# Kernel tuning notes

Hardware: AMD Instinct MI355X
Metric: run time of the kernel (lower is better)

## Reference

```python
import jax, jax.numpy as jnp
import numpy as np

CAPACITY_FACTOR = 1.0  # fairseq Top1Gate default


def setup_inputs() -> dict:
    key = jax.random.key(0)
    ks = jax.random.split(key, 5)
    B, T, M, H, O, E = 8, 1024, 1024, 4096, 1024, 4
    return {
        "hidden_states": jax.random.normal(ks[0], (B, T, M), jnp.float32),
        "gate_w": jax.random.normal(ks[1], (M, E), jnp.float32) * 0.02,
        "fc1_w": jax.random.normal(ks[2], (E, M, H), jnp.float32) * 0.02,
        "fc1_b": jnp.zeros((E, H), jnp.float32),
        "fc2_w": jax.random.normal(ks[3], (E, H, O), jnp.float32) * 0.02,
        "fc2_b": jnp.zeros((E, O), jnp.float32),
    }


def reference(hidden_states, gate_w, fc1_w, fc1_b, fc2_w, fc2_b):
    B, T, M = hidden_states.shape
    E = gate_w.shape[1]
    S = B * T
    C = int(CAPACITY_FACTOR * -(-S // E))  # ceil(S/E)

    features = hidden_states.reshape(S, M)  # [S, M]

    # ---- Top1 gate (fairseq top1gating, eval path: no shuffle/noise) ----
    logits = features @ gate_w                      # [S, E]
    gates = jax.nn.softmax(logits, axis=1)          # [S, E]
    idx = jnp.argmax(gates, axis=1)                 # [S]
    mask1 = jax.nn.one_hot(idx, E, dtype=gates.dtype)  # [S, E]

    # load-balancing aux loss (computed before capacity dropping)
    me = jnp.mean(gates, axis=0)
    ce = jnp.mean(mask1, axis=0)
    l_aux = jnp.sum(me * ce) * E

    # capacity: position within each expert's queue; drop overflow tokens
    locations = jnp.cumsum(mask1, axis=0) - 1.0     # [S, E]
    mask1 = mask1 * (locations < C)
    loc_s = jnp.sum(locations * mask1, axis=1).astype(jnp.int32)  # [S]
    gates1_s = jnp.sum(gates * mask1, axis=1)       # [S] gate value (0 if dropped)

    # combine_weights [S, E, C] and boolean dispatch mask (as float for mm)
    combine = (gates1_s[:, None, None] * mask1[:, :, None]
               * jax.nn.one_hot(loc_s, C, dtype=gates.dtype)[:, None, :])
    dispatch = (combine > 0).astype(features.dtype)  # [S, E, C]

    # ---- dispatch via dense one-hot matmul: [E*C, S] @ [S, M] ----
    dispatch_ecs = jnp.transpose(dispatch, (1, 2, 0)).reshape(E * C, S)
    dispatched = (dispatch_ecs @ features).reshape(E, C, M)

    # ---- per-expert MLP (grouped GEMM) ----
    h = jax.nn.gelu(jnp.einsum('ecm,emh->ech', dispatched, fc1_w) + fc1_b[:, None, :])
    expert_out = jnp.einsum('ech,eho->eco', h, fc2_w) + fc2_b[:, None, :]  # [E, C, O]

    # ---- combine via dense matmul: [S, E*C] @ [E*C, O] ----
    O = expert_out.shape[-1]
    combined = combine.reshape(S, E * C) @ expert_out.reshape(E * C, O)

    return combined.reshape(B, T, O), l_aux
```

## Files before the change

### kernel.cpp

```cpp
#include <hip/hip_runtime.h>
#include <stdint.h>

#define S_TOK 8192
#define MDIM  1024
#define HDIM  4096
#define ODIM  1024
#define NEXP  4
#define CAP   2048

typedef __attribute__((ext_vector_type(8))) short short8;
typedef __attribute__((ext_vector_type(4))) float floatx4;

__device__ __forceinline__ unsigned short f2bf(float x) {
  union { float f; unsigned u; } v; v.f = x;
  unsigned r = v.u + 0x7FFFu + ((v.u >> 16) & 1u);
  return (unsigned short)(r >> 16);
}

__device__ __forceinline__ void gl_lds16(const void* g, void* l) {
  __builtin_amdgcn_global_load_lds(
      (const __attribute__((address_space(1))) void*)g,
      (__attribute__((address_space(3))) void*)l, 16, 0, 0);
}

__device__ __forceinline__ float gelu_tanh(float x) {
  float z = 0.7978845608028654f * (x + 0.044715f * x * x * x);
  float t = 1.0f - 2.0f / (__expf(2.0f * z) + 1.0f);
  return 0.5f * x * (1.0f + t);
}

__global__ __launch_bounds__(256) void gate_kernel(
    const float* __restrict__ feat, const float* __restrict__ gw,
    int* __restrict__ idx, float* __restrict__ gval, float* __restrict__ gsum)
{
  int wave = threadIdx.x >> 6, lane = threadIdx.x & 63;
  int s = blockIdx.x * 4 + wave;
  const float* f = feat + (size_t)s * MDIM;
  double a0 = 0, a1 = 0, a2 = 0, a3 = 0;
  #pragma unroll
  for (int j = 0; j < 16; ++j) {
    int m = lane + j * 64;
    float x = f[m];
    float4 w = ((const float4*)gw)[m];
    a0 += (double)x * w.x; a1 += (double)x * w.y;
    a2 += (double)x * w.z; a3 += (double)x * w.w;
  }
  #pragma unroll
  for (int off = 32; off; off >>= 1) {
    a0 += __shfl_down(a0, off); a1 += __shfl_down(a1, off);
    a2 += __shfl_down(a2, off); a3 += __shfl_down(a3, off);
  }
  __shared__ float bs[4];
  if (threadIdx.x < 4) bs[threadIdx.x] = 0.f;
  __syncthreads();
  if (lane == 0) {
    double lg[4] = {a0, a1, a2, a3};
    double mx = lg[0]; int bi = 0;
    #pragma unroll
    for (int e = 1; e < 4; ++e) if (lg[e] > mx) { mx = lg[e]; bi = e; }
    float ex[4]; float den = 0.f;
    #pragma unroll
    for (int e = 0; e < 4; ++e) { ex[e] = __expf((float)(lg[e] - mx)); den += ex[e]; }
    float inv = 1.f / den;
    idx[s]  = bi;
    gval[s] = ex[bi] * inv;
    #pragma unroll
    for (int e = 0; e < 4; ++e) atomicAdd(&bs[e], ex[e] * inv);
  }
  __syncthreads();
  if (threadIdx.x < 4) atomicAdd(&gsum[threadIdx.x], bs[threadIdx.x]);
}

__global__ __launch_bounds__(1024) void scan_kernel(
    const int* __restrict__ idx, int* __restrict__ perm,
    int* __restrict__ ne, const float* __restrict__ gsum,
    float* __restrict__ laux)
{
  const int tid = threadIdx.x, wave = tid >> 6, lane = tid & 63;
  __shared__ int cnt[16][4];
  __shared__ int off[16][4];
  __shared__ int tot[4];
  unsigned long long below = (lane == 0) ? 0ull : ((~0ull) >> (64 - lane));

  int myE[8], loc[8];
  int c[4] = {0, 0, 0, 0};
  #pragma unroll
  for (int j = 0; j < 8; ++j) {
    int s = wave * 512 + j * 64 + lane;
    int ev = idx[s];
    myE[j] = ev;
    #pragma unroll
    for (int e = 0; e < 4; ++e) {
      unsigned long long mb = __ballot(ev == e);
      if (ev == e) loc[j] = c[e] + __popcll(mb & below);
      c[e] += __popcll(mb);
    }
  }
  if (lane == 0) {
    #pragma unroll
    for (int e = 0; e < 4; ++e) cnt[wave][e] = c[e];
  }
  __syncthreads();
  if (tid < 64) {
    int w = tid >> 2, e = tid & 3;
    int o = 0;
    for (int w2 = 0; w2 < 16; ++w2) if (w2 < w) o += cnt[w2][e];
    off[w][e] = o;
    if (w == 15) tot[e] = o + cnt[15][e];
  }
  __syncthreads();
  #pragma unroll
  for (int j = 0; j < 8; ++j) {
    int s = wave * 512 + j * 64 + lane;
    int e = myE[j];
    int rank = off[wave][e] + loc[j];
    if (rank < CAP) perm[e * CAP + rank] = s;
  }
  if (tid < 4) ne[tid] = tot[tid] < CAP ? tot[tid] : CAP;
  if (tid == 0) {
    float l = 0.f;
    #pragma unroll
    for (int e = 0; e < 4; ++e)
      l += (gsum[e] * (1.0f / S_TOK)) * ((float)tot[e] * (1.0f / S_TOK));
    *laux = l * (float)NEXP;
  }
}

__global__ __launch_bounds__(256) void transpose_cast(
    const float* __restrict__ in, unsigned short* __restrict__ out, int R, int Cc)
{
  __shared__ unsigned short tile[64][66];
  in  += (size_t)blockIdx.z * R * Cc;
  out += (size_t)blockIdx.z * R * Cc;
  int c0 = blockIdx.x * 64, r0 = blockIdx.y * 64;
  int tx = threadIdx.x & 15;
  int ty = threadIdx.x >> 4;
  #pragma unroll
  for (int p = 0; p < 4; ++p) {
    int r = ty + p * 16;
    float4 v = *(const float4*)(in + (size_t)(r0 + r) * Cc + c0 + tx * 4);
    tile[r][tx * 4 + 0] = f2bf(v.x);
    tile[r][tx * 4 + 1] = f2bf(v.y);
    tile[r][tx * 4 + 2] = f2bf(v.z);
    tile[r][tx * 4 + 3] = f2bf(v.w);
  }
  __syncthreads();
  #pragma unroll
  for (int p = 0; p < 4; ++p) {
    int c = ty + p * 16;
    ushort4 o;
    o.x = tile[tx * 4 + 0][c];
    o.y = tile[tx * 4 + 1][c];
    o.z = tile[tx * 4 + 2][c];
    o.w = tile[tx * 4 + 3][c];
    *(ushort4*)(out + (size_t)(c0 + c) * R + r0 + tx * 4) = o;
  }
}

__global__ __launch_bounds__(256) void gather_kernel(
    const float* __restrict__ feat, const int* __restrict__ perm,
    const int* __restrict__ ne, unsigned short* __restrict__ disp)
{
  int b = blockIdx.x;
  int e = b >> 11, c = b & (CAP - 1);
  int m = threadIdx.x * 4;
  ushort4 o;
  if (c < ne[e]) {
    int s = perm[b];
    float4 v = *(const float4*)(feat + (size_t)s * MDIM + m);
    o.x = f2bf(v.x); o.y = f2bf(v.y); o.z = f2bf(v.z); o.w = f2bf(v.w);
  } else {
    o.x = o.y = o.z = o.w = 0;
  }
  *(ushort4*)(disp + (size_t)b * MDIM + m) = o;
}

__global__ __launch_bounds__(256) void fc1_kernel(
    const unsigned short* __restrict__ A, const unsigned short* __restrict__ Bt,
    const float* __restrict__ b1, unsigned short* __restrict__ Hb)
{
  const int e = blockIdx.z, nb = blockIdx.x, mb = blockIdx.y;
  const int tid = threadIdx.x, wave = tid >> 6, lane = tid & 63;

  __shared__ __align__(16) unsigned short smA[128 * 32];
  __shared__ __align__(16) unsigned short smB[128 * 32];

  const char* Ag = (const char*)(A + ((size_t)e * CAP + (size_t)mb * 128) * MDIM);
  const char* Bg = (const char*)(Bt + ((size_t)e * HDIM + (size_t)nb * 128) * MDIM);

  int boff0 = (wave * 2 + 0) * 1024 + lane * 16;
  int boff1 = (wave * 2 + 1) * 1024 + lane * 16;
  const char* agp0 = Ag + (size_t)(boff0 >> 6) * 2048 + (boff0 & 63);
  const char* agp1 = Ag + (size_t)(boff1 >> 6) * 2048 + (boff1 & 63);
  const char* bgp0 = Bg + (size_t)(boff0 >> 6) * 2048 + (boff0 & 63);
  const char* bgp1 = Bg + (size_t)(boff1 >> 6) * 2048 + (boff1 & 63);
  unsigned short* sA0 = smA + (wave * 2 + 0) * 512;
  unsigned short* sA1 = smA + (wave * 2 + 1) * 512;
  unsigned short* sB0 = smB + (wave * 2 + 0) * 512;
  unsigned short* sB1 = smB + (wave * 2 + 1) * 512;

  const int wm = (wave & 1) * 64, wn = (wave >> 1) * 64;
  const int fr = lane & 15, fq = lane >> 4;

  floatx4 acc[4][4] = {};

  for (int kt = 0; kt < MDIM / 32; ++kt) {
    int kb = kt * 64;
    gl_lds16(agp0 + kb, sA0);
    gl_lds16(agp1 + kb, sA1);
    gl_lds16(bgp0 + kb, sB0);
    gl_lds16(bgp1 + kb, sB1);
    __syncthreads();
    short8 af[4], bfr[4];
    #pragma unroll
    for (int i = 0; i < 4; ++i)
      af[i] = *(const short8*)&smA[(wm + i * 16 + fr) * 32 + fq * 8];
    #pragma unroll
    for (int j = 0; j < 4; ++j)
      bfr[j] = *(const short8*)&smB[(wn + j * 16 + fr) * 32 + fq * 8];
    #pragma unroll
    for (int i = 0; i < 4; ++i)
      #pragma unroll
      for (int j = 0; j < 4; ++j)
        acc[i][j] = __builtin_amdgcn_mfma_f32_16x16x32_bf16(af[i], bfr[j], acc[i][j], 0, 0, 0);
    __syncthreads();
  }

  unsigned short* Hrow = Hb + (size_t)e * CAP * HDIM;
  #pragma unroll
  for (int j = 0; j < 4; ++j) {
    int gn = nb * 128 + wn + j * 16 + fr;
    float bv = b1[e * HDIM + gn];
    #pragma unroll
    for (int i = 0; i < 4; ++i) {
      int m0 = mb * 128 + wm + i * 16 + fq * 4;
      #pragma unroll
      for (int r = 0; r < 4; ++r)
        Hrow[(size_t)(m0 + r) * HDIM + gn] = f2bf(gelu_tanh(acc[i][j][r] + bv));
    }
  }
}

__global__ __launch_bounds__(256) void fc2_kernel(
    const unsigned short* __restrict__ A, const unsigned short* __restrict__ Bt,
    const float* __restrict__ b2, const int* __restrict__ perm,
    const int* __restrict__ ne, const float* __restrict__ gval,
    float* __restrict__ out)
{
  const int b = blockIdx.x;
  const int wg = (b & 7) * 128 + (b >> 3);
  const int nb = wg & 7, mb = (wg >> 3) & 31, e = wg >> 8;
  const int tid = threadIdx.x, wave = tid >> 6, lane = tid & 63;

  __shared__ __align__(16) unsigned short smA[3 * 64 * 32];
  __shared__ __align__(16) unsigned short smB[3 * 128 * 32];

  const char* Ag = (const char*)(A + ((size_t)e * CAP + (size_t)mb * 64) * HDIM);
  const char* Bg = (const char*)(Bt + ((size_t)e * ODIM + (size_t)nb * 128) * HDIM);

  int boffA = tid * 16;
  const char* agp = Ag + (size_t)(boffA >> 6) * 8192 + (boffA & 63);
  int boff0 = (wave * 2 + 0) * 1024 + lane * 16;
  int boff1 = (wave * 2 + 1) * 1024 + lane * 16;
  const char* bgp0 = Bg + (size_t)(boff0 >> 6) * 8192 + (boff0 & 63);
  const char* bgp1 = Bg + (size_t)(boff1 >> 6) * 8192 + (boff1 & 63);

  const int ldsA_w = wave * 512;
  const int ldsB_w0 = (wave * 2 + 0) * 512;
  const int ldsB_w1 = (wave * 2 + 1) * 512;

  const int wm = (wave & 1) * 32, wn = (wave >> 1) * 64;
  const int fr = lane & 15, fq = lane >> 4;

  floatx4 acc[2][4] = {};

  const int NT = HDIM / 32;
  int c0 = 0, c1 = 1, c2 = 2;

  {
    gl_lds16(agp + 0 * 64,  smA + 0 * 2048 + ldsA_w);
    gl_lds16(bgp0 + 0 * 64, smB + 0 * 4096 + ldsB_w0);
    gl_lds16(bgp1 + 0 * 64, smB + 0 * 4096 + ldsB_w1);
    gl_lds16(agp + 1 * 64,  smA + 1 * 2048 + ldsA_w);
    gl_lds16(bgp0 + 1 * 64, smB + 1 * 4096 + ldsB_w0);
    gl_lds16(bgp1 + 1 * 64, smB + 1 * 4096 + ldsB_w1);
  }
  asm volatile("s_waitcnt vmcnt(3)" ::: "memory");
  __builtin_amdgcn_s_barrier();

  for (int kt = 0; kt < NT; ++kt) {
    if (kt + 2 < NT) {
      int kb = (kt + 2) * 64;
      gl_lds16(agp + kb,  smA + c2 * 2048 + ldsA_w);
      gl_lds16(bgp0 + kb, smB + c2 * 4096 + ldsB_w0);
      gl_lds16(bgp1 + kb, smB + c2 * 4096 + ldsB_w1);
    }
    const unsigned short* sA = smA + c0 * 2048;
    const unsigned short* sB = smB + c0 * 4096;
    short8 af[2], bfr[4];
    #pragma unroll
    for (int i = 0; i < 2; ++i)
      af[i] = *(const short8*)&sA[(wm + i * 16 + fr) * 32 + fq * 8];
    #pragma unroll
    for (int j = 0; j < 4; ++j)
      bfr[j] = *(const short8*)&sB[(wn + j * 16 + fr) * 32 + fq * 8];
    #pragma unroll
    for (int i = 0; i < 2; ++i)
      #pragma unroll
      for (int j = 0; j < 4; ++j)
        acc[i][j] = __builtin_amdgcn_mfma_f32_16x16x32_bf16(af[i], bfr[j], acc[i][j], 0, 0, 0);
    if (kt + 1 < NT) {
      if (kt + 2 < NT) asm volatile("s_waitcnt vmcnt(3)" ::: "memory");
      else             asm volatile("s_waitcnt vmcnt(0)" ::: "memory");
      __builtin_amdgcn_s_barrier();
    }
    int t = c0; c0 = c1; c1 = c2; c2 = t;
  }

  const int nE = ne[e];
  float b2v[4];
  #pragma unroll
  for (int j = 0; j < 4; ++j)
    b2v[j] = b2[e * ODIM + nb * 128 + wn + j * 16 + fr];
  #pragma unroll
  for (int i = 0; i < 2; ++i) {
    #pragma unroll
    for (int r = 0; r < 4; ++r) {
      int c = mb * 64 + wm + i * 16 + fq * 4 + r;
      if (c < nE) {
        int s = perm[e * CAP + c];
        float g = gval[s];
        float* orow = out + (size_t)s * ODIM + nb * 128 + wn;
        #pragma unroll
        for (int j = 0; j < 4; ++j)
          orow[j * 16 + fr] = (acc[i][j][r] + b2v[j]) * g;
      }
    }
  }
}

extern "C" void kernel_launch(void* const* d_in, const int* in_sizes, int n_in,
                              void* d_out, int out_size, void* d_ws, size_t ws_size,
                              hipStream_t stream) {
  const float* feat = (const float*)d_in[0];
  const float* gw   = (const float*)d_in[1];
  const float* w1   = (const float*)d_in[2];
  const float* b1   = (const float*)d_in[3];
  const float* w2   = (const float*)d_in[4];
  const float* b2   = (const float*)d_in[5];
  float* out = (float*)d_out;

  char* ws = (char*)d_ws;
  unsigned short* wt   = (unsigned short*)(ws);
  unsigned short* hbuf = (unsigned short*)(ws + 33554432);
  unsigned short* disp = (unsigned short*)(ws + 100663296);
  int*   idx  = (int*)  (ws + 117440512);
  float* gval = (float*)(ws + 117473280);
  int*   perm = (int*)  (ws + 117506048);
  float* gsum = (float*)(ws + 117538816);
  int*   ne   = (int*)  (ws + 117538832);

  hipMemsetAsync(d_out, 0, (size_t)S_TOK * ODIM * sizeof(float), stream);
  hipMemsetAsync(ws + 117538816, 0, 32, stream);

  gate_kernel<<<S_TOK / 4, 256, 0, stream>>>(feat, gw, idx, gval, gsum);
  scan_kernel<<<1, 1024, 0, stream>>>(idx, perm, ne, gsum, out + (size_t)S_TOK * ODIM);
  transpose_cast<<<dim3(HDIM / 64, MDIM / 64, NEXP), 256, 0, stream>>>(w1, wt, MDIM, HDIM);
  gather_kernel<<<NEXP * CAP, 256, 0, stream>>>(feat, perm, ne, disp);
  fc1_kernel<<<dim3(HDIM / 128, CAP / 128, NEXP), 256, 0, stream>>>(disp, wt, b1, hbuf);
  transpose_cast<<<dim3(ODIM / 64, HDIM / 64, NEXP), 256, 0, stream>>>(w2, wt, HDIM, ODIM);
  fc2_kernel<<<1024, 256, 0, stream>>>(hbuf, wt, b2, perm, ne, gval, out);
}
```

Measured before the change: 431.4 us.

## Triple-buffer fc1 loads, XOR-swizzle LDS tiles, and remap fc1 workgroups per XCD

The fc1 GEMM goes from a single-buffered loop with two barriers per k-step to a three-stage global_load_lds pipeline using vmcnt waits and one barrier, the scheme fc2 already uses. Both GEMMs now write their LDS tiles with an XOR swizzle of the 16-byte column slot and read fragments with the matching swizzle, to cut LDS bank conflicts. fc1 also moves to a 1D grid with a block index remap that groups neighbouring tiles on the same XCD for better L2 reuse. The cost is three times the LDS per fc1 block, which may lower occupancy.

```diff
diff --git a/kernel.cpp b/kernel.cpp
--- a/kernel.cpp
+++ b/kernel.cpp
@@ -27,6 +27,14 @@
   float z = 0.7978845608028654f * (x + 0.044715f * x * x * x);
   float t = 1.0f - 2.0f / (__expf(2.0f * z) + 1.0f);
   return 0.5f * x * (1.0f + t);
+}
+
+__device__ __forceinline__ const char* stage_src(const char* base, int linoff,
+                                                 int rowstride) {
+  int row  = linoff >> 6;
+  int slot = (linoff >> 4) & 3;
+  int c16  = slot ^ ((row >> 1) & 3);
+  return base + (size_t)row * rowstride + (c16 << 4);
 }
 
 __global__ __launch_bounds__(256) void gate_kernel(
@@ -179,51 +187,75 @@
     const unsigned short* __restrict__ A, const unsigned short* __restrict__ Bt,
     const float* __restrict__ b1, unsigned short* __restrict__ Hb)
 {
-  const int e = blockIdx.z, nb = blockIdx.x, mb = blockIdx.y;
+  const int b = blockIdx.x;
+  const int wg = (b & 7) * 256 + (b >> 3);
+  const int nb = wg & 31, mb = (wg >> 5) & 15, e = wg >> 9;
   const int tid = threadIdx.x, wave = tid >> 6, lane = tid & 63;
 
-  __shared__ __align__(16) unsigned short smA[128 * 32];
-  __shared__ __align__(16) unsigned short smB[128 * 32];
+  __shared__ __align__(16) unsigned short smA[3 * 128 * 32];
+  __shared__ __align__(16) unsigned short smB[3 * 128 * 32];
 
   const char* Ag = (const char*)(A + ((size_t)e * CAP + (size_t)mb * 128) * MDIM);
   const char* Bg = (const char*)(Bt + ((size_t)e * HDIM + (size_t)nb * 128) * MDIM);
 
-  int boff0 = (wave * 2 + 0) * 1024 + lane * 16;
-  int boff1 = (wave * 2 + 1) * 1024 + lane * 16;
-  const char* agp0 = Ag + (size_t)(boff0 >> 6) * 2048 + (boff0 & 63);
-  const char* agp1 = Ag + (size_t)(boff1 >> 6) * 2048 + (boff1 & 63);
-  const char* bgp0 = Bg + (size_t)(boff0 >> 6) * 2048 + (boff0 & 63);
-  const char* bgp1 = Bg + (size_t)(boff1 >> 6) * 2048 + (boff1 & 63);
-  unsigned short* sA0 = smA + (wave * 2 + 0) * 512;
-  unsigned short* sA1 = smA + (wave * 2 + 1) * 512;
-  unsigned short* sB0 = smB + (wave * 2 + 0) * 512;
-  unsigned short* sB1 = smB + (wave * 2 + 1) * 512;
+  const int boff0 = (wave * 2 + 0) * 1024 + lane * 16;
+  const int boff1 = (wave * 2 + 1) * 1024 + lane * 16;
+  const char* agp0 = stage_src(Ag, boff0, 2048);
+  const char* agp1 = stage_src(Ag, boff1, 2048);
+  const char* bgp0 = stage_src(Bg, boff0, 2048);
+  const char* bgp1 = stage_src(Bg, boff1, 2048);
+  const int ldsw0 = (wave * 2 + 0) * 512;
+  const int ldsw1 = (wave * 2 + 1) * 512;
 
   const int wm = (wave & 1) * 64, wn = (wave >> 1) * 64;
   const int fr = lane & 15, fq = lane >> 4;
+  const int sqA = ((fq ^ ((wm + fr) >> 1)) & 3) * 8;
+  const int sqB = ((fq ^ ((wn + fr) >> 1)) & 3) * 8;
 
   floatx4 acc[4][4] = {};
 
-  for (int kt = 0; kt < MDIM / 32; ++kt) {
-    int kb = kt * 64;
-    gl_lds16(agp0 + kb, sA0);
-    gl_lds16(agp1 + kb, sA1);
-    gl_lds16(bgp0 + kb, sB0);
-    gl_lds16(bgp1 + kb, sB1);
-    __syncthreads();
+  const int NT = MDIM / 32;
+  int c0 = 0, c1 = 1, c2 = 2;
+
+  gl_lds16(agp0 + 0,  smA + 0 * 4096 + ldsw0);
+  gl_lds16(agp1 + 0,  smA + 0 * 4096 + ldsw1);
+  gl_lds16(bgp0 + 0,  smB + 0 * 4096 + ldsw0);
+  gl_lds16(bgp1 + 0,  smB + 0 * 4096 + ldsw1);
+  gl_lds16(agp0 + 64, smA + 1 * 4096 + ldsw0);
+  gl_lds16(agp1 + 64, smA + 1 * 4096 + ldsw1);
+  gl_lds16(bgp0 + 64, smB + 1 * 4096 + ldsw0);
+  gl_lds16(bgp1 + 64, smB + 1 * 4096 + ldsw1);
+  asm volatile("s_waitcnt vmcnt(4)" ::: "memory");
+  __builtin_amdgcn_s_barrier();
+
+  for (int kt = 0; kt < NT; ++kt) {
+    if (kt + 2 < NT) {
+      int kb = (kt + 2) * 64;
+      gl_lds16(agp0 + kb, smA + c2 * 4096 + ldsw0);
+      gl_lds16(agp1 + kb, smA + c2 * 4096 + ldsw1);
+      gl_lds16(bgp0 + kb, smB + c2 * 4096 + ldsw0);
+      gl_lds16(bgp1 + kb, smB + c2 * 4096 + ldsw1);
+    }
+    const unsigned short* sA = smA + c0 * 4096;
+    const unsigned short* sB = smB + c0 * 4096;
     short8 af[4], bfr[4];
     #pragma unroll
     for (int i = 0; i < 4; ++i)
-      af[i] = *(const short8*)&smA[(wm + i * 16 + fr) * 32 + fq * 8];
+      af[i] = *(const short8*)&sA[(wm + i * 16 + fr) * 32 + sqA];
     #pragma unroll
     for (int j = 0; j < 4; ++j)
-      bfr[j] = *(const short8*)&smB[(wn + j * 16 + fr) * 32 + fq * 8];
+      bfr[j] = *(const short8*)&sB[(wn + j * 16 + fr) * 32 + sqB];
     #pragma unroll
     for (int i = 0; i < 4; ++i)
       #pragma unroll
       for (int j = 0; j < 4; ++j)
         acc[i][j] = __builtin_amdgcn_mfma_f32_16x16x32_bf16(af[i], bfr[j], acc[i][j], 0, 0, 0);
-    __syncthreads();
+    if (kt + 1 < NT) {
+      if (kt + 2 < NT) asm volatile("s_waitcnt vmcnt(4)" ::: "memory");
+      else             asm volatile("s_waitcnt vmcnt(0)" ::: "memory");
+      __builtin_amdgcn_s_barrier();
+    }
+    int t = c0; c0 = c1; c1 = c2; c2 = t;
   }
 
   unsigned short* Hrow = Hb + (size_t)e * CAP * HDIM;
@@ -258,12 +290,11 @@
   const char* Ag = (const char*)(A + ((size_t)e * CAP + (size_t)mb * 64) * HDIM);
   const char* Bg = (const char*)(Bt + ((size_t)e * ODIM + (size_t)nb * 128) * HDIM);
 
-  int boffA = tid * 16;
-  const char* agp = Ag + (size_t)(boffA >> 6) * 8192 + (boffA & 63);
-  int boff0 = (wave * 2 + 0) * 1024 + lane * 16;
-  int boff1 = (wave * 2 + 1) * 1024 + lane * 16;
-  const char* bgp0 = Bg + (size_t)(boff0 >> 6) * 8192 + (boff0 & 63);
-  const char* bgp1 = Bg + (size_t)(boff1 >> 6) * 8192 + (boff1 & 63);
+  const char* agp = stage_src(Ag, tid * 16, 8192);
+  const int boff0 = (wave * 2 + 0) * 1024 + lane * 16;
+  const int boff1 = (wave * 2 + 1) * 1024 + lane * 16;
+  const char* bgp0 = stage_src(Bg, boff0, 8192);
+  const char* bgp1 = stage_src(Bg, boff1, 8192);
 
   const int ldsA_w = wave * 512;
   const int ldsB_w0 = (wave * 2 + 0) * 512;
@@ -271,20 +302,20 @@
 
   const int wm = (wave & 1) * 32, wn = (wave >> 1) * 64;
   const int fr = lane & 15, fq = lane >> 4;
+  const int sqA = ((fq ^ ((wm + fr) >> 1)) & 3) * 8;
+  const int sqB = ((fq ^ ((wn + fr) >> 1)) & 3) * 8;
 
   floatx4 acc[2][4] = {};
 
   const int NT = HDIM / 32;
   int c0 = 0, c1 = 1, c2 = 2;
 
-  {
-    gl_lds16(agp + 0 * 64,  smA + 0 * 2048 + ldsA_w);
-    gl_lds16(bgp0 + 0 * 64, smB + 0 * 4096 + ldsB_w0);
-    gl_lds16(bgp1 + 0 * 64, smB + 0 * 4096 + ldsB_w1);
-    gl_lds16(agp + 1 * 64,  smA + 1 * 2048 + ldsA_w);
-    gl_lds16(bgp0 + 1 * 64, smB + 1 * 4096 + ldsB_w0);
-    gl_lds16(bgp1 + 1 * 64, smB + 1 * 4096 + ldsB_w1);
-  }
+  gl_lds16(agp + 0 * 64,  smA + 0 * 2048 + ldsA_w);
+  gl_lds16(bgp0 + 0 * 64, smB + 0 * 4096 + ldsB_w0);
+  gl_lds16(bgp1 + 0 * 64, smB + 0 * 4096 + ldsB_w1);
+  gl_lds16(agp + 1 * 64,  smA + 1 * 2048 + ldsA_w);
+  gl_lds16(bgp0 + 1 * 64, smB + 1 * 4096 + ldsB_w0);
+  gl_lds16(bgp1 + 1 * 64, smB + 1 * 4096 + ldsB_w1);
   asm volatile("s_waitcnt vmcnt(3)" ::: "memory");
   __builtin_amdgcn_s_barrier();
 
@@ -300,10 +331,10 @@
     short8 af[2], bfr[4];
     #pragma unroll
     for (int i = 0; i < 2; ++i)
-      af[i] = *(const short8*)&sA[(wm + i * 16 + fr) * 32 + fq * 8];
+      af[i] = *(const short8*)&sA[(wm + i * 16 + fr) * 32 + sqA];
     #pragma unroll
     for (int j = 0; j < 4; ++j)
-      bfr[j] = *(const short8*)&sB[(wn + j * 16 + fr) * 32 + fq * 8];
+      bfr[j] = *(const short8*)&sB[(wn + j * 16 + fr) * 32 + sqB];
     #pragma unroll
     for (int i = 0; i < 2; ++i)
       #pragma unroll
@@ -367,7 +398,7 @@
   scan_kernel<<<1, 1024, 0, stream>>>(idx, perm, ne, gsum, out + (size_t)S_TOK * ODIM);
   transpose_cast<<<dim3(HDIM / 64, MDIM / 64, NEXP), 256, 0, stream>>>(w1, wt, MDIM, HDIM);
   gather_kernel<<<NEXP * CAP, 256, 0, stream>>>(feat, perm, ne, disp);
-  fc1_kernel<<<dim3(HDIM / 128, CAP / 128, NEXP), 256, 0, stream>>>(disp, wt, b1, hbuf);
+  fc1_kernel<<<2048, 256, 0, stream>>>(disp, wt, b1, hbuf);
   transpose_cast<<<dim3(ODIM / 64, HDIM / 64, NEXP), 256, 0, stream>>>(w2, wt, HDIM, ODIM);
   fc2_kernel<<<1024, 256, 0, stream>>>(hbuf, wt, b2, perm, ne, gval, out);
 }
```

Measured after the change: 442.4 us. 2.5% more time.
